# Performance work log

Hardware: AMD Instinct MI355X
Metric: run time of the kernel (lower is better)

Reference implementation:

```python
import jax, jax.numpy as jnp
import numpy as np

HIDDEN = 2048
N_HEADS = 16
HEAD_DIM = HIDDEN // N_HEADS  # 128
GROUP_SIZE = 128
ROPE_THETA = 10000.0
EPS = 1e-8
THRESH = 0.5


def ternary_quantize_groupwise(w):
    O, I = w.shape
    wg = w.reshape(O, I // GROUP_SIZE, GROUP_SIZE)
    scale = jnp.maximum(jnp.mean(jnp.abs(wg), axis=-1, keepdims=True), EPS)
    wn = wg / scale
    q = jnp.where(wn > THRESH, 1.0, jnp.where(wn < -THRESH, -1.0, 0.0))
    return (q * scale).reshape(O, I)


def quantize_with_ste(w):
    wq = ternary_quantize_groupwise(w)
    return w + jax.lax.stop_gradient(wq - w)


def rope_tables(seqlen):
    half = HEAD_DIM // 2
    inv_freq = 1.0 / (ROPE_THETA ** (jnp.arange(half, dtype=jnp.float32) / half))
    freqs = jnp.arange(seqlen, dtype=jnp.float32)[:, None] * inv_freq[None, :]  # [S, half]
    return jnp.cos(freqs), jnp.sin(freqs)


def apply_rope(x, cos, sin):
    # x: [B, H, S, D]; cos/sin: [S, D/2]
    d = x.shape[-1]
    x1, x2 = x[..., : d // 2], x[..., d // 2:]
    c = cos[None, None, :, :].astype(x.dtype)
    s = sin[None, None, :, :].astype(x.dtype)
    return jnp.concatenate([x1 * c - x2 * s, x1 * s + x2 * c], axis=-1)


def setup_inputs() -> dict:
    key = jax.random.key(0)
    ks = jax.random.split(key, 5)
    B, S = 1, 2048
    hidden_states = jax.random.normal(ks[0], (B, S, HIDDEN), dtype=jnp.float32)
    attention_mask = jnp.ones((B, S), dtype=jnp.int32)
    init_scale = 1.0 / np.sqrt(HIDDEN)
    wq = jax.random.normal(ks[1], (HIDDEN, HIDDEN), dtype=jnp.float32) * init_scale
    wk = jax.random.normal(ks[2], (HIDDEN, HIDDEN), dtype=jnp.float32) * init_scale
    wv = jax.random.normal(ks[3], (HIDDEN, HIDDEN), dtype=jnp.float32) * init_scale
    wo = jax.random.normal(ks[4], (HIDDEN, HIDDEN), dtype=jnp.float32) * init_scale
    return {"hidden_states": hidden_states, "attention_mask": attention_mask,
            "wq": wq, "wk": wk, "wv": wv, "wo": wo}


def reference(hidden_states, attention_mask, wq, wk, wv, wo):
    B, S, _ = hidden_states.shape
    cos, sin = rope_tables(S)

    def proj(x, w):
        w_q = quantize_with_ste(w)
        y = jnp.einsum('bsi,oi->bso', x, w_q)
        return y.reshape(B, S, N_HEADS, HEAD_DIM).transpose(0, 2, 1, 3)  # [B,H,S,D]

    q = apply_rope(proj(hidden_states, wq), cos, sin)
    k = apply_rope(proj(hidden_states, wk), cos, sin)
    v = proj(hidden_states, wv)

    scores = jnp.einsum('bhsd,bhtd->bhst', q, k) / np.sqrt(HEAD_DIM)
    causal = jnp.triu(jnp.ones((S, S), dtype=bool), k=1)
    scores = jnp.where(causal[None, None, :, :], -jnp.inf, scores)
    pad = (attention_mask == 0)[:, None, None, :]
    scores = jnp.where(pad, -jnp.inf, scores)

    probs = jax.nn.softmax(scores, axis=-1)
    out = jnp.einsum('bhst,bhtd->bhsd', probs, v)
    out = out.transpose(0, 2, 1, 3).reshape(B, S, HIDDEN)

    wo_q = quantize_with_ste(wo)
    return jnp.einsum('bso,po->bsp', out, wo_q)
```

## Files before the change

kernel.cpp:

```cpp
#include <hip/hip_runtime.h>
#include <cstdint>
#include <cstddef>


typedef __attribute__((ext_vector_type(8))) short bf16x8;
typedef __attribute__((ext_vector_type(4))) float f32x4;
typedef __attribute__((address_space(3))) void lds_void;
typedef const __attribute__((address_space(1))) void gmem_void;

__device__ __forceinline__ short f2bf(float x) {
    union { float f; uint32_t u; } c; c.f = x;
    uint32_t r = (c.u + 0x7FFFu + ((c.u >> 16) & 1u)) >> 16;
    return (short)r;
}
__device__ __forceinline__ float bf2f(short x) {
    union { uint32_t u; float f; } c; c.u = ((uint32_t)(uint16_t)x) << 16;
    return c.f;
}

__global__ __launch_bounds__(64) void zero_flag(int* f) {
    if (threadIdx.x == 0) *f = 0;
}

__global__ __launch_bounds__(256) void detect_kernel(
    const unsigned short* __restrict__ p, int n, int* __restrict__ flag)
{
    int tid = blockIdx.x * 256 + threadIdx.x;
    int cnt = 0;
    for (int i = tid; i < n; i += 65536) {
        int e = (p[i] >> 7) & 0xFF;
        cnt += (e >= 0xF0) ? 1 : 0;
    }
#pragma unroll
    for (int off = 1; off < 64; off <<= 1) cnt += __shfl_xor(cnt, off);
    if ((threadIdx.x & 63) == 0 && cnt) atomicAdd(flag, cnt);
}

__global__ __launch_bounds__(256) void convert_kernel(
    const void* __restrict__ in, short* __restrict__ out, int n,
    const int* __restrict__ flag)
{
    bool isf32 = (*flag > 1000);
    int i = blockIdx.x * 256 + threadIdx.x;
    if (i >= n) return;
    out[i] = isf32 ? f2bf(((const float*)in)[i]) : ((const short*)in)[i];
}

__global__ __launch_bounds__(256) void quant_kernel(
    const void* __restrict__ w0, const void* __restrict__ w1,
    const void* __restrict__ w2, const void* __restrict__ w3,
    short* __restrict__ q0, short* __restrict__ q1,
    short* __restrict__ q2, short* __restrict__ q3,
    const int* __restrict__ flag)
{
    bool isf32 = (*flag > 1000);
    int gw   = blockIdx.x * 4 + (threadIdx.x >> 6);
    int lane = threadIdx.x & 63;
    int mat  = gw >> 15;
    int g    = gw & 32767;
    const void* w = (mat == 0) ? w0 : (mat == 1) ? w1 : (mat == 2) ? w2 : w3;
    short*      q = (mat == 0) ? q0 : (mat == 1) ? q1 : (mat == 2) ? q2 : q3;
    int idx = g * 64 + lane;
    float a, b;
    if (isf32) {
        const float* wf = (const float*)w;
        a = wf[idx * 2]; b = wf[idx * 2 + 1];
    } else {
        int pr = ((const int*)w)[idx];
        a = bf2f((short)(pr & 0xFFFF));
        b = bf2f((short)(((uint32_t)pr) >> 16));
    }
    float s = fabsf(a) + fabsf(b);
#pragma unroll
    for (int off = 1; off < 64; off <<= 1) s += __shfl_xor(s, off);
    float scale = fmaxf(s * (1.0f / 128.0f), 1e-8f);
    float na = a / scale, nb = b / scale;
    float ra = (na > 0.5f) ? scale : (na < -0.5f) ? -scale : 0.0f;
    float rb = (nb > 0.5f) ? scale : (nb < -0.5f) ? -scale : 0.0f;
    ((int*)q)[idx] = (int)(uint16_t)f2bf(ra) | ((int)(uint16_t)f2bf(rb) << 16);
}

__global__ __launch_bounds__(256) void gemm_qkv(
    const short* __restrict__ A, const short* __restrict__ B,
    short* __restrict__ Cqk, short* __restrict__ Cv)
{
    int bx = blockIdx.x, by = blockIdx.y;
    const short* Ab = A + (long long)by * 128 * 2048;
    const short* Bb = B + (long long)bx * 128 * 2048;
    __shared__ short lA[128 * 64];
    __shared__ short lB[128 * 64];
    int tid = threadIdx.x;
    int lane = tid & 63, wv = tid >> 6;
    f32x4 acc[4][4];
#pragma unroll
    for (int i = 0; i < 4; i++)
#pragma unroll
        for (int j = 0; j < 4; j++)
#pragma unroll
            for (int r = 0; r < 4; r++) acc[i][j][r] = 0.0f;

    int rbase = (wv >> 1) * 64, cbase = (wv & 1) * 64;

    for (int k0 = 0; k0 < 2048; k0 += 64) {
        __syncthreads();
#pragma unroll
        for (int i = 0; i < 4; i++) {
            int ci  = i * 256 + tid;
            int row = ci >> 3;
            int kcG = (ci & 7) ^ (row & 7);
            const short* gp = Ab + (long long)row * 2048 + k0 + kcG * 8;
            __builtin_amdgcn_global_load_lds((gmem_void*)gp, (lds_void*)(lA + ci * 8), 16, 0, 0);
        }
#pragma unroll
        for (int i = 0; i < 4; i++) {
            int ci  = i * 256 + tid;
            int row = ci >> 3;
            int kcG = (ci & 7) ^ (row & 7);
            const short* gp = Bb + (long long)row * 2048 + k0 + kcG * 8;
            __builtin_amdgcn_global_load_lds((gmem_void*)gp, (lds_void*)(lB + ci * 8), 16, 0, 0);
        }
        __syncthreads();
#pragma unroll
        for (int kk = 0; kk < 2; kk++) {
            int kc = kk * 4 + (lane >> 4);
            bf16x8 a[4], b[4];
#pragma unroll
            for (int t = 0; t < 4; t++) {
                int r = rbase + t * 16 + (lane & 15);
                a[t] = *(const bf16x8*)(lA + (r * 8 + (kc ^ (r & 7))) * 8);
            }
#pragma unroll
            for (int t = 0; t < 4; t++) {
                int r = cbase + t * 16 + (lane & 15);
                b[t] = *(const bf16x8*)(lB + (r * 8 + (kc ^ (r & 7))) * 8);
            }
#pragma unroll
            for (int mt = 0; mt < 4; mt++)
#pragma unroll
                for (int nt = 0; nt < 4; nt++)
                    acc[mt][nt] = __builtin_amdgcn_mfma_f32_16x16x32_bf16(a[mt], b[nt], acc[mt][nt], 0, 0, 0);
        }
    }

    int rq = (lane >> 4) * 4, cq = lane & 15;
    if (bx < 32) {
#pragma unroll
        for (int mt = 0; mt < 4; mt++)
#pragma unroll
            for (int nt = 0; nt < 4; nt++)
#pragma unroll
                for (int r = 0; r < 4; r++) {
                    int row = by * 128 + rbase + mt * 16 + rq + r;
                    int col = bx * 128 + cbase + nt * 16 + cq;
                    Cqk[(long long)row * 4096 + col] = f2bf(acc[mt][nt][r]);
                }
    } else {
#pragma unroll
        for (int mt = 0; mt < 4; mt++)
#pragma unroll
            for (int nt = 0; nt < 4; nt++)
#pragma unroll
                for (int r = 0; r < 4; r++) {
                    int row = by * 128 + rbase + mt * 16 + rq + r;
                    int colv = (bx - 32) * 128 + cbase + nt * 16 + cq;
                    Cv[(long long)colv * 2048 + row] = f2bf(acc[mt][nt][r]);
                }
    }
}

__global__ __launch_bounds__(256) void gemm_wo(
    const short* __restrict__ A, const short* __restrict__ B,
    float* __restrict__ C)
{
    int bx = blockIdx.x, by = blockIdx.y;
    const short* Ab = A + (long long)by * 128 * 2048;
    const short* Bb = B + (long long)bx * 64 * 2048;
    __shared__ short lA[128 * 64];
    __shared__ short lB[64 * 64];
    int tid = threadIdx.x;
    int lane = tid & 63, wv = tid >> 6;
    f32x4 acc[2][4];
#pragma unroll
    for (int i = 0; i < 2; i++)
#pragma unroll
        for (int j = 0; j < 4; j++)
#pragma unroll
            for (int r = 0; r < 4; r++) acc[i][j][r] = 0.0f;

    int rbase = wv * 32;

    for (int k0 = 0; k0 < 2048; k0 += 64) {
        __syncthreads();
#pragma unroll
        for (int i = 0; i < 4; i++) {
            int ci  = i * 256 + tid;
            int row = ci >> 3;
            int kcG = (ci & 7) ^ (row & 7);
            const short* gp = Ab + (long long)row * 2048 + k0 + kcG * 8;
            __builtin_amdgcn_global_load_lds((gmem_void*)gp, (lds_void*)(lA + ci * 8), 16, 0, 0);
        }
#pragma unroll
        for (int i = 0; i < 2; i++) {
            int ci  = i * 256 + tid;
            int row = ci >> 3;
            int kcG = (ci & 7) ^ (row & 7);
            const short* gp = Bb + (long long)row * 2048 + k0 + kcG * 8;
            __builtin_amdgcn_global_load_lds((gmem_void*)gp, (lds_void*)(lB + ci * 8), 16, 0, 0);
        }
        __syncthreads();
#pragma unroll
        for (int kk = 0; kk < 2; kk++) {
            int kc = kk * 4 + (lane >> 4);
            bf16x8 a[2], b[4];
#pragma unroll
            for (int t = 0; t < 2; t++) {
                int r = rbase + t * 16 + (lane & 15);
                a[t] = *(const bf16x8*)(lA + (r * 8 + (kc ^ (r & 7))) * 8);
            }
#pragma unroll
            for (int t = 0; t < 4; t++) {
                int r = t * 16 + (lane & 15);
                b[t] = *(const bf16x8*)(lB + (r * 8 + (kc ^ (r & 7))) * 8);
            }
#pragma unroll
            for (int mt = 0; mt < 2; mt++)
#pragma unroll
                for (int nt = 0; nt < 4; nt++)
                    acc[mt][nt] = __builtin_amdgcn_mfma_f32_16x16x32_bf16(a[mt], b[nt], acc[mt][nt], 0, 0, 0);
        }
    }

    int rq = (lane >> 4) * 4, cq = lane & 15;
#pragma unroll
    for (int mt = 0; mt < 2; mt++)
#pragma unroll
        for (int nt = 0; nt < 4; nt++)
#pragma unroll
            for (int r = 0; r < 4; r++) {
                int row = by * 128 + rbase + mt * 16 + rq + r;
                int col = bx * 64 + nt * 16 + cq;
                C[(long long)row * 2048 + col] = acc[mt][nt][r];
            }
}

__global__ __launch_bounds__(256) void rope_kernel(
    const short* __restrict__ qk,
    short* __restrict__ qr, short* __restrict__ kr)
{
    int idx = blockIdx.x * 256 + threadIdx.x;
    int d = idx & 63;
    int h = (idx >> 6) & 15;
    int s = idx >> 10;
    float inv = exp2f((float)d * -0.20762050593261719f);
    float ang = (float)s * inv;
    float sn, c;
    sincosf(ang, &sn, &c);
    long long io = (long long)s * 4096 + h * 128 + d;
    long long oo = (long long)h * 262144 + (long long)s * 128 + d;
    float x1 = bf2f(qk[io]), x2 = bf2f(qk[io + 64]);
    qr[oo]      = f2bf(x1 * c - x2 * sn);
    qr[oo + 64] = f2bf(x1 * sn + x2 * c);
    x1 = bf2f(qk[io + 2048]); x2 = bf2f(qk[io + 2112]);
    kr[oo]      = f2bf(x1 * c - x2 * sn);
    kr[oo + 64] = f2bf(x1 * sn + x2 * c);
}

__global__ __launch_bounds__(256) void flash_kernel(
    const short* __restrict__ q_r, const short* __restrict__ k_r,
    const short* __restrict__ v_t, float* __restrict__ Opart,
    float* __restrict__ mpart, float* __restrict__ lpart)
{
    const float SC = 0.08838834764831845f;
    int bid = blockIdx.x;
    int qt = 31 - (bid >> 5);
    int h  = (bid >> 1) & 15;
    int z  = bid & 1;
    int n  = qt + 1;
    int jhalf = (n + 1) >> 1;
    int jb = z ? jhalf : 0;
    int je = z ? n : jhalf;

    int tid = threadIdx.x, lane = tid & 63, wv = tid >> 6;
    int quad = lane >> 4, lm = lane & 15;

    __shared__ short lK[64 * 128];
    __shared__ short lV[128 * 64];
    __shared__ short lP[64 * 64];

    const short* qb = q_r + h * 262144 + (qt * 64 + wv * 16) * 128;
    const short* kb = k_r + h * 262144;
    const short* vb = v_t + h * 128 * 2048;

    bf16x8 aq[4];
#pragma unroll
    for (int kc = 0; kc < 4; kc++)
        aq[kc] = *(const bf16x8*)(qb + lm * 128 + kc * 32 + quad * 8);

    f32x4 ao[8];
#pragma unroll
    for (int nt = 0; nt < 8; nt++)
#pragma unroll
        for (int r = 0; r < 4; r++) ao[nt][r] = 0.0f;
    float mrow[4], lrow[4];
#pragma unroll
    for (int r = 0; r < 4; r++) { mrow[r] = -1e30f; lrow[r] = 0.0f; }

    if (jb < je) {
#pragma unroll
        for (int i = 0; i < 4; i++) {
            int ci = i * 256 + tid;
            int r = ci >> 4, cp = ci & 15;
            int c = (cp & 8) | ((cp & 7) ^ (r & 7));
            const short* gp = kb + (jb * 64 + r) * 128 + c * 8;
            __builtin_amdgcn_global_load_lds((gmem_void*)gp, (lds_void*)(lK + ci * 8), 16, 0, 0);
        }
    }
    __syncthreads();

    for (int jt = jb; jt < je; jt++) {
#pragma unroll
        for (int i = 0; i < 4; i++) {
            int ci = i * 256 + tid;
            int r = ci >> 3, cp = ci & 7;
            int c = cp ^ (r & 7);
            const short* gp = vb + r * 2048 + jt * 64 + c * 8;
            __builtin_amdgcn_global_load_lds((gmem_void*)gp, (lds_void*)(lV + ci * 8), 16, 0, 0);
        }
        f32x4 as[4];
#pragma unroll
        for (int nt = 0; nt < 4; nt++)
#pragma unroll
            for (int r = 0; r < 4; r++) as[nt][r] = 0.0f;
#pragma unroll
        for (int kc = 0; kc < 4; kc++) {
#pragma unroll
            for (int nt = 0; nt < 4; nt++) {
                int r = nt * 16 + lm;
                int c = kc * 4 + quad;
                int slot = (c & 8) | ((c & 7) ^ (r & 7));
                bf16x8 bk = *(const bf16x8*)(lK + (r * 16 + slot) * 8);
                as[nt] = __builtin_amdgcn_mfma_f32_16x16x32_bf16(aq[kc], bk, as[nt], 0, 0, 0);
            }
        }
        bool diag = (jt == qt);
#pragma unroll
        for (int nt = 0; nt < 4; nt++)
#pragma unroll
            for (int r = 0; r < 4; r++) {
                float s = as[nt][r] * SC;
                if (diag) {
                    int qg = wv * 16 + quad * 4 + r;
                    int tg = nt * 16 + lm;
                    if (tg > qg) s = -1e30f;
                }
                as[nt][r] = s;
            }
#pragma unroll
        for (int r = 0; r < 4; r++) {
            float mx = fmaxf(fmaxf(as[0][r], as[1][r]), fmaxf(as[2][r], as[3][r]));
#pragma unroll
            for (int off = 1; off < 16; off <<= 1) mx = fmaxf(mx, __shfl_xor(mx, off));
            float mnew = fmaxf(mrow[r], mx);
            float alpha = __expf(mrow[r] - mnew);
            mrow[r] = mnew;
            float psum = 0.0f;
#pragma unroll
            for (int nt = 0; nt < 4; nt++) {
                float p = __expf(as[nt][r] - mnew);
                as[nt][r] = p;
                psum += p;
            }
#pragma unroll
            for (int off = 1; off < 16; off <<= 1) psum += __shfl_xor(psum, off);
            lrow[r] = lrow[r] * alpha + psum;
#pragma unroll
            for (int nt = 0; nt < 8; nt++) ao[nt][r] *= alpha;
            int row = wv * 16 + quad * 4 + r;
#pragma unroll
            for (int nt = 0; nt < 4; nt++) {
                int slot = (nt * 2 + (lm >> 3) + row) & 7;
                lP[row * 64 + slot * 8 + (lm & 7)] = f2bf(as[nt][r]);
            }
        }
        __syncthreads();
        if (jt + 1 < je) {
#pragma unroll
            for (int i = 0; i < 4; i++) {
                int ci = i * 256 + tid;
                int r = ci >> 4, cp = ci & 15;
                int c = (cp & 8) | ((cp & 7) ^ (r & 7));
                const short* gp = kb + ((jt + 1) * 64 + r) * 128 + c * 8;
                __builtin_amdgcn_global_load_lds((gmem_void*)gp, (lds_void*)(lK + ci * 8), 16, 0, 0);
            }
        }
#pragma unroll
        for (int kt = 0; kt < 2; kt++) {
            int prow = wv * 16 + lm;
            int slot = (kt * 4 + quad + prow) & 7;
            bf16x8 ap = *(const bf16x8*)(lP + prow * 64 + slot * 8);
#pragma unroll
            for (int nt = 0; nt < 8; nt++) {
                int r = nt * 16 + lm;
                int c = kt * 4 + quad;
                int vslot = c ^ (r & 7);
                bf16x8 bv = *(const bf16x8*)(lV + (r * 8 + vslot) * 8);
                ao[nt] = __builtin_amdgcn_mfma_f32_16x16x32_bf16(ap, bv, ao[nt], 0, 0, 0);
            }
        }
        __syncthreads();
    }
    float* Ob = Opart + (long long)z * 4194304;
#pragma unroll
    for (int r = 0; r < 4; r++) {
        int sg = qt * 64 + wv * 16 + quad * 4 + r;
#pragma unroll
        for (int nt = 0; nt < 8; nt++) {
            int dg = h * 128 + nt * 16 + lm;
            Ob[(long long)sg * 2048 + dg] = ao[nt][r];
        }
        if (lm == 0) {
            mpart[z * 32768 + h * 2048 + sg] = mrow[r];
            lpart[z * 32768 + h * 2048 + sg] = lrow[r];
        }
    }
}

__global__ __launch_bounds__(256) void combine_kernel(
    const float* __restrict__ O0, const float* __restrict__ O1,
    const float* __restrict__ mpart, const float* __restrict__ lpart,
    short* __restrict__ attn)
{
    int idx = blockIdx.x * 256 + threadIdx.x;
    int e = idx * 4;
    int s = e >> 11, h = (e & 2047) >> 7;
    float m0 = mpart[h * 2048 + s], m1 = mpart[32768 + h * 2048 + s];
    float l0 = lpart[h * 2048 + s], l1 = lpart[32768 + h * 2048 + s];
    float M = fmaxf(m0, m1);
    float w0 = __expf(m0 - M), w1 = __expf(m1 - M);
    float inv = 1.0f / (l0 * w0 + l1 * w1);
    float4 a = *(const float4*)(O0 + e);
    float4 b = *(const float4*)(O1 + e);
    short4 o;
    o.x = f2bf((a.x * w0 + b.x * w1) * inv);
    o.y = f2bf((a.y * w0 + b.y * w1) * inv);
    o.z = f2bf((a.z * w0 + b.z * w1) * inv);
    o.w = f2bf((a.w * w0 + b.w * w1) * inv);
    *(short4*)(attn + e) = o;
}

extern "C" void kernel_launch(void* const* d_in, const int* in_sizes, int n_in,
                              void* d_out, int out_size, void* d_ws, size_t ws_size,
                              hipStream_t stream)
{
    const void* x  = d_in[0];
    const void* wq = d_in[2];
    const void* wk = d_in[3];
    const void* wv = d_in[4];
    const void* wo = d_in[5];

    char* ws = (char*)d_ws;
    size_t off = 0;
    auto alloc = [&](size_t b) { void* p = ws + off; off += (b + 255) & ~(size_t)255; return p; };
    short* wqkv_q = (short*)alloc(25165824);
    short* wo_q   = (short*)alloc(8388608);
    short* qk     = (short*)alloc(16777216);
    short* v_t    = (short*)alloc(8388608);
    short* q_r    = (short*)alloc(8388608);
    short* k_r    = (short*)alloc(8388608);
    short* attn   = (short*)alloc(8388608);
    short* x_bf   = (short*)alloc(8388608);
    float* Opart  = (float*)alloc(33554432);
    float* mpart  = (float*)alloc(262144);
    float* lpart  = (float*)alloc(262144);
    int*   flag   = (int*)alloc(256);
    if (off > ws_size) return;

    zero_flag<<<1, 64, 0, stream>>>(flag);
    detect_kernel<<<256, 256, 0, stream>>>(
        (const unsigned short*)x, in_sizes[0], flag);
    convert_kernel<<<16384, 256, 0, stream>>>(x, x_bf, 4194304, flag);

    quant_kernel<<<32768, 256, 0, stream>>>(wq, wk, wv, wo,
        wqkv_q, wqkv_q + 4194304, wqkv_q + 8388608, wo_q, flag);

    gemm_qkv<<<dim3(48,16), 256, 0, stream>>>(x_bf, wqkv_q, qk, v_t);

    rope_kernel<<<8192, 256, 0, stream>>>(qk, q_r, k_r);

    flash_kernel<<<1024, 256, 0, stream>>>(q_r, k_r, v_t, Opart, mpart, lpart);
    combine_kernel<<<4096, 256, 0, stream>>>(
        Opart, Opart + 4194304, mpart, lpart, attn);

    gemm_wo<<<dim3(32,16), 256, 0, stream>>>(attn, wo_q, (float*)d_out);
}
```

Measured before the change: 333.9 us.

## Vectorize input conversion, stage V-transpose stores via LDS, reswizzle P tile

The input conversion kernel now handles four elements per thread with vector loads and stores, and launches a quarter as many blocks. The V-output transpose in the QKV GEMM is staged through reused, XOR-swizzled shared memory so global writes become contiguous 16-byte stores instead of scattered 2-byte ones. The swizzle of the P tile in the flash kernel is changed so its shared-memory writes and reads hit fewer bank conflicts. These target uncoalesced global stores and LDS conflicts, at the cost of two extra barriers in the V path.

```diff
diff --git a/kernel.cpp b/kernel.cpp
--- a/kernel.cpp
+++ b/kernel.cpp
@@ -41,9 +41,16 @@
     const int* __restrict__ flag)
 {
     bool isf32 = (*flag > 1000);
-    int i = blockIdx.x * 256 + threadIdx.x;
+    int i = (blockIdx.x * 256 + threadIdx.x) * 4;
     if (i >= n) return;
-    out[i] = isf32 ? f2bf(((const float*)in)[i]) : ((const short*)in)[i];
+    if (isf32) {
+        float4 v = *(const float4*)((const float*)in + i);
+        short4 o;
+        o.x = f2bf(v.x); o.y = f2bf(v.y); o.z = f2bf(v.z); o.w = f2bf(v.w);
+        *(short4*)(out + i) = o;
+    } else {
+        *(short4*)(out + i) = *(const short4*)((const short*)in + i);
+    }
 }
 
 __global__ __launch_bounds__(256) void quant_kernel(
@@ -87,8 +94,9 @@
     int bx = blockIdx.x, by = blockIdx.y;
     const short* Ab = A + (long long)by * 128 * 2048;
     const short* Bb = B + (long long)bx * 128 * 2048;
-    __shared__ short lA[128 * 64];
-    __shared__ short lB[128 * 64];
+    __shared__ short ls[16384];
+    short* lA = ls;
+    short* lB = ls + 8192;
     int tid = threadIdx.x;
     int lane = tid & 63, wv = tid >> 6;
     f32x4 acc[4][4];
@@ -155,16 +163,28 @@
                     Cqk[(long long)row * 4096 + col] = f2bf(acc[mt][nt][r]);
                 }
     } else {
+        __syncthreads();
 #pragma unroll
         for (int mt = 0; mt < 4; mt++)
 #pragma unroll
             for (int nt = 0; nt < 4; nt++)
 #pragma unroll
                 for (int r = 0; r < 4; r++) {
-                    int row = by * 128 + rbase + mt * 16 + rq + r;
-                    int colv = (bx - 32) * 128 + cbase + nt * 16 + cq;
-                    Cv[(long long)colv * 2048 + row] = f2bf(acc[mt][nt][r]);
+                    int row = rbase + mt * 16 + rq + r;
+                    int col = cbase + nt * 16 + cq;
+                    int rcs = (row >> 3) ^ (col & 15);
+                    ls[col * 128 + rcs * 8 + (row & 7)] = f2bf(acc[mt][nt][r]);
                 }
+        __syncthreads();
+        int o = tid >> 1, half = tid & 1;
+        long long og = (long long)((bx - 32) * 128 + o) * 2048 + by * 128;
+#pragma unroll
+        for (int c = 0; c < 8; c++) {
+            int ch = half * 8 + c;
+            int chs = ch ^ (o & 15);
+            bf16x8 v = *(const bf16x8*)(ls + o * 128 + chs * 8);
+            *(bf16x8*)(Cv + og + ch * 8) = v;
+        }
     }
 }
 
@@ -378,7 +398,7 @@
             int row = wv * 16 + quad * 4 + r;
 #pragma unroll
             for (int nt = 0; nt < 4; nt++) {
-                int slot = (nt * 2 + (lm >> 3) + row) & 7;
+                int slot = (nt * 2 + (lm >> 3) + 2 * quad) & 7;
                 lP[row * 64 + slot * 8 + (lm & 7)] = f2bf(as[nt][r]);
             }
         }
@@ -396,7 +416,7 @@
 #pragma unroll
         for (int kt = 0; kt < 2; kt++) {
             int prow = wv * 16 + lm;
-            int slot = (kt * 4 + quad + prow) & 7;
+            int slot = (kt * 4 + quad + 2 * (lm >> 2)) & 7;
             bf16x8 ap = *(const bf16x8*)(lP + prow * 64 + slot * 8);
 #pragma unroll
             for (int nt = 0; nt < 8; nt++) {
@@ -478,7 +498,7 @@
     zero_flag<<<1, 64, 0, stream>>>(flag);
     detect_kernel<<<256, 256, 0, stream>>>(
         (const unsigned short*)x, in_sizes[0], flag);
-    convert_kernel<<<16384, 256, 0, stream>>>(x, x_bf, 4194304, flag);
+    convert_kernel<<<4096, 256, 0, stream>>>(x, x_bf, 4194304, flag);
 
     quant_kernel<<<32768, 256, 0, stream>>>(wq, wk, wv, wo,
         wqkv_q, wqkv_q + 4194304, wqkv_q + 8388608, wo_q, flag);
```

After: 332.6 us. No clear change (-0.4%).
